# Kernel optimization log

Hardware: AMD Instinct MI355X
Metric: run time of the kernel (lower is better)

## Reference

```python
import jax, jax.numpy as jnp
import numpy as np

D = 1024      # embed_size
H = 16        # num_heads
NEXP = 8      # num_experts
TOPK = 3
THRESH = 0.05
COEF = 0.01
B, SQ, SKV = 4, 1024, 1024


def _ln(x, g, b, eps=1e-5):
    m = jnp.mean(x, axis=-1, keepdims=True)
    v = jnp.mean(jnp.square(x - m), axis=-1, keepdims=True)
    return (x - m) * jax.lax.rsqrt(v + eps) * g + b


def setup_inputs() -> dict:
    key = jax.random.key(0)
    ks = jax.random.split(key, 20)
    s = 0.02
    w = lambda k, shape: (jax.random.normal(k, shape, jnp.float32) * s)
    return {
        'query': jax.random.normal(ks[0], (B, SQ, D), jnp.float32),
        'key_value': jax.random.normal(ks[1], (B, SKV, D), jnp.float32),
        'Wq': w(ks[2], (D, D)), 'bq': jnp.zeros((D,), jnp.float32),
        'Wk': w(ks[3], (D, D)), 'bk': jnp.zeros((D,), jnp.float32),
        'Wv': w(ks[4], (D, D)), 'bv': jnp.zeros((D,), jnp.float32),
        'W_in': w(ks[5], (3 * D, D)), 'b_in': jnp.zeros((3 * D,), jnp.float32),
        'W_out': w(ks[6], (D, D)), 'b_out': jnp.zeros((D,), jnp.float32),
        'Wa': w(ks[7], (D, D)), 'ba': jnp.zeros((D,), jnp.float32),
        'ln1_g': jnp.ones((D,), jnp.float32), 'ln1_b': jnp.zeros((D,), jnp.float32),
        'Wg': w(ks[8], (D, NEXP)),
        'ew1': w(ks[9], (NEXP, D, 4 * D)), 'eb1': jnp.zeros((NEXP, 4 * D), jnp.float32),
        'ew2': w(ks[10], (NEXP, 4 * D, D)), 'eb2': jnp.zeros((NEXP, D), jnp.float32),
        'ln2_g': jnp.ones((D,), jnp.float32), 'ln2_b': jnp.zeros((D,), jnp.float32),
    }


def reference(query, key_value, Wq, bq, Wk, bk, Wv, bv, W_in, b_in, W_out, b_out,
              Wa, ba, ln1_g, ln1_b, Wg, ew1, eb1, ew2, eb2, ln2_g, ln2_b):
    Bq, Sq, _ = query.shape
    Skv = key_value.shape[1]
    Dh = D // H
    # outer Q/K/V linears (torch Linear: x @ W.T + b)
    q = query @ Wq.T + bq
    k = key_value @ Wk.T + bk
    v = key_value @ Wv.T + bv
    # nn.MultiheadAttention in-projection
    Wiq, Wik, Wiv = jnp.split(W_in, 3, axis=0)
    biq, bik, biv = jnp.split(b_in, 3)
    qh = (q @ Wiq.T + biq).reshape(Bq, Sq, H, Dh).transpose(0, 2, 1, 3)
    kh = (k @ Wik.T + bik).reshape(Bq, Skv, H, Dh).transpose(0, 2, 1, 3)
    vh = (v @ Wiv.T + biv).reshape(Bq, Skv, H, Dh).transpose(0, 2, 1, 3)
    scores = jnp.einsum('bhqd,bhkd->bhqk', qh, kh) / jnp.sqrt(jnp.float32(Dh))
    attn = jax.nn.softmax(scores, axis=-1)
    o = jnp.einsum('bhqk,bhkd->bhqd', attn, vh).transpose(0, 2, 1, 3).reshape(Bq, Sq, D)
    o = o @ W_out.T + b_out
    # adapt + residual + first_norm
    x = _ln(o @ Wa.T + ba + query, ln1_g, ln1_b)
    # ---- MoE: top-3 softmax gating, threshold on non-top-1 gates ----
    probs = jax.nn.softmax(x @ Wg, axis=-1)                 # [B,S,E]
    topv, topi = jax.lax.top_k(probs, TOPK)                  # [B,S,3]
    keep = jnp.concatenate([jnp.ones_like(topv[..., :1], bool),
                            topv[..., 1:] >= THRESH], axis=-1)
    topv = jnp.where(keep, topv, 0.0)
    combine = jnp.sum(jax.nn.one_hot(topi, NEXP, dtype=x.dtype) * topv[..., None], axis=-2)  # [B,S,E]
    moe_out = jnp.zeros_like(x)
    for e in range(NEXP):  # small fixed expert count
        h = jax.nn.gelu(x @ ew1[e] + eb1[e], approximate=False)
        moe_out = moe_out + combine[..., e:e + 1] * (h @ ew2[e] + eb2[e])
    # load-balance aux loss: E * sum(frac_routed * mean_prob) * coef
    fe = jnp.mean((combine > 0).astype(x.dtype), axis=(0, 1))
    me = jnp.mean(probs, axis=(0, 1))
    aux = COEF * NEXP * jnp.sum(fe * me)
    out = _ln(moe_out + x, ln2_g, ln2_b)
    return out, aux
```

## Files before the change

### kernel.cpp

```cpp
#include <hip/hip_runtime.h>
#include <math.h>

#define THRESH_C 0.05f
#define COEF_C   0.01f

typedef __bf16 bf16;
typedef __bf16 bf16x8 __attribute__((ext_vector_type(8)));
typedef __bf16 bf16x4 __attribute__((ext_vector_type(4)));
typedef float  f32x4  __attribute__((ext_vector_type(4)));

__device__ __forceinline__ void ld16(void* lds_base, const void* g) {
    __builtin_amdgcn_global_load_lds(
        (const __attribute__((address_space(1))) void*)g,
        (__attribute__((address_space(3))) void*)lds_base,
        16, 0, 0);
}

__device__ __forceinline__ int xcd_swz(int orig, int nwg) {
    int q = nwg >> 3, r = nwg & 7;
    int xcd = orig & 7, idx = orig >> 3;
    return (xcd < r ? xcd * (q + 1) : r * (q + 1) + (xcd - r) * q) + idx;
}

__global__ __launch_bounds__(256) void k_f32_to_split(const float* __restrict__ in,
                                                      bf16* __restrict__ hi,
                                                      bf16* __restrict__ lo, long n) {
    long i = ((long)blockIdx.x * 256 + threadIdx.x) * 4;
    if (i >= n) return;
    float4 v = *(const float4*)(in + i);
    bf16x4 h, l;
    h[0] = (bf16)v.x; l[0] = (bf16)(v.x - (float)h[0]);
    h[1] = (bf16)v.y; l[1] = (bf16)(v.y - (float)h[1]);
    h[2] = (bf16)v.z; l[2] = (bf16)(v.z - (float)h[2]);
    h[3] = (bf16)v.w; l[3] = (bf16)(v.w - (float)h[3]);
    *(bf16x4*)(hi + i) = h;
    *(bf16x4*)(lo + i) = l;
}

__global__ __launch_bounds__(256) void k_transpose4_split(const float* __restrict__ w0,
                                                          const float* __restrict__ w1,
                                                          const float* __restrict__ w2,
                                                          const float* __restrict__ w3,
                                                          bf16* __restrict__ oh,
                                                          bf16* __restrict__ ol) {
    __shared__ float t[64][65];
    int z = blockIdx.z;
    const float* in = (z == 0) ? w0 : (z == 1) ? w1 : (z == 2) ? w2 : w3;
    bf16* ohz = oh + (long)z * 1048576;
    bf16* olz = ol + (long)z * 1048576;
    int r0 = blockIdx.y * 64, c0 = blockIdx.x * 64;
    for (int i = threadIdx.x; i < 4096; i += 256) {
        int r = i >> 6, c = i & 63;
        t[r][c] = in[(long)(r0 + r) * 1024 + (c0 + c)];
    }
    __syncthreads();
    for (int i = threadIdx.x; i < 4096; i += 256) {
        int c = i >> 6, r = i & 63;
        float v = t[r][c];
        bf16 h = (bf16)v;
        long o = (long)(c0 + c) * 1024 + (r0 + r);
        ohz[o] = h;
        olz[o] = (bf16)(v - (float)h);
    }
}

__global__ __launch_bounds__(256) void k_transpose_ew(const float* __restrict__ in,
                                                      bf16* __restrict__ out,
                                                      int R, int C) {
    __shared__ bf16 t[64][65];
    const float* ib = in + (long)blockIdx.z * R * C;
    bf16* ob = out + (long)blockIdx.z * R * C;
    int r0 = blockIdx.y * 64, c0 = blockIdx.x * 64;
    for (int i = threadIdx.x; i < 4096; i += 256) {
        int r = i >> 6, c = i & 63;
        t[r][c] = (bf16)ib[(long)(r0 + r) * C + (c0 + c)];
    }
    __syncthreads();
    for (int i = threadIdx.x; i < 4096; i += 256) {
        int c = i >> 6, r = i & 63;
        ob[(long)(c0 + c) * R + (r0 + r)] = t[r][c];
    }
}

__global__ __launch_bounds__(256) void k_bias_fold4(const float* __restrict__ W_in,
                                                    const float* __restrict__ Wa,
                                                    const float* __restrict__ bq,
                                                    const float* __restrict__ bk,
                                                    const float* __restrict__ bv,
                                                    const float* __restrict__ b_out,
                                                    const float* __restrict__ b_in,
                                                    const float* __restrict__ ba,
                                                    float* __restrict__ y) {
    int z = blockIdx.y;
    const float* W  = (z < 3) ? (W_in + (long)z * 1048576) : Wa;
    const float* b1 = (z == 0) ? bq : (z == 1) ? bk : (z == 2) ? bv : b_out;
    const float* b2 = (z < 3) ? (b_in + z * 1024) : ba;
    int row = blockIdx.x * 4 + (threadIdx.x >> 6);
    int lane = threadIdx.x & 63;
    const float* wr = W + (long)row * 1024;
    float s = 0.f;
    for (int k = lane; k < 1024; k += 64) s += wr[k] * b1[k];
#pragma unroll
    for (int o = 32; o >= 1; o >>= 1) s += __shfl_xor(s, o);
    if (lane == 0) y[z * 1024 + row] = b2[row] + s;
}

enum { HP_SPLIT = 0, HP_F32 = 1, HP_SPLIT_HEADS = 2 };

template<int MODE>
__global__ __launch_bounds__(256)
void gemm_hp(const bf16* __restrict__ Ah, const bf16* __restrict__ Al, int lda, long sAz,
             const bf16* __restrict__ Bh, const bf16* __restrict__ Bl, int ldb, long sBz,
             void* __restrict__ Chv, bf16* __restrict__ Cl, int ldc, long sCz,
             const float* __restrict__ bias, float alpha, int M, int N, int K) {
    __shared__ alignas(16) bf16 sAh[128 * 32];
    __shared__ alignas(16) bf16 sAl[128 * 32];
    __shared__ alignas(16) bf16 sBh[128 * 32];
    __shared__ alignas(16) bf16 sBl[128 * 32];
    const int bm = blockIdx.y, bn = blockIdx.x, z = blockIdx.z;
    const int tid  = threadIdx.x;
    const int lane = tid & 63, wave = tid >> 6;
    const int quad = lane >> 4, l16 = lane & 15;
    const int wr = wave >> 1, wc = wave & 1;
    const int sr = tid >> 2;
    const int sc = (tid & 3) * 8;

    int arow0 = min(bm * 128 + sr, M - 1);
    int arow1 = min(bm * 128 + sr + 64, M - 1);
    int brow0 = min(bn * 128 + sr, N - 1);
    int brow1 = min(bn * 128 + sr + 64, N - 1);

    const bf16* pAh0 = Ah + (long)z * sAz + (long)arow0 * lda + sc;
    const bf16* pAh1 = Ah + (long)z * sAz + (long)arow1 * lda + sc;
    const bf16* pAl0 = Al + (long)z * sAz + (long)arow0 * lda + sc;
    const bf16* pAl1 = Al + (long)z * sAz + (long)arow1 * lda + sc;
    const bf16* pBh0 = Bh + (long)z * sBz + (long)brow0 * ldb + sc;
    const bf16* pBh1 = Bh + (long)z * sBz + (long)brow1 * ldb + sc;
    const bf16* pBl0 = Bl + (long)z * sBz + (long)brow0 * ldb + sc;
    const bf16* pBl1 = Bl + (long)z * sBz + (long)brow1 * ldb + sc;
    const int wo = wave << 9;

    f32x4 acc[4][4];
#pragma unroll
    for (int i = 0; i < 4; i++)
#pragma unroll
        for (int j = 0; j < 4; j++) acc[i][j] = (f32x4){0.f, 0.f, 0.f, 0.f};

    for (int k0 = 0; k0 < K; k0 += 32) {
        __syncthreads();
        ld16(sAh + wo,        pAh0 + k0);
        ld16(sAh + 2048 + wo, pAh1 + k0);
        ld16(sAl + wo,        pAl0 + k0);
        ld16(sAl + 2048 + wo, pAl1 + k0);
        ld16(sBh + wo,        pBh0 + k0);
        ld16(sBh + 2048 + wo, pBh1 + k0);
        ld16(sBl + wo,        pBl0 + k0);
        ld16(sBl + 2048 + wo, pBl1 + k0);
        __syncthreads();
        bf16x8 ah[4], al[4], bh[4], bl[4];
#pragma unroll
        for (int i = 0; i < 4; i++) {
            int ro = (wr * 64 + i * 16 + l16) * 32 + quad * 8;
            ah[i] = *(const bf16x8*)&sAh[ro];
            al[i] = *(const bf16x8*)&sAl[ro];
        }
#pragma unroll
        for (int j = 0; j < 4; j++) {
            int ro = (wc * 64 + j * 16 + l16) * 32 + quad * 8;
            bh[j] = *(const bf16x8*)&sBh[ro];
            bl[j] = *(const bf16x8*)&sBl[ro];
        }
#pragma unroll
        for (int i = 0; i < 4; i++)
#pragma unroll
            for (int j = 0; j < 4; j++) {
                acc[i][j] = __builtin_amdgcn_mfma_f32_16x16x32_bf16(al[i], bh[j], acc[i][j], 0, 0, 0);
                acc[i][j] = __builtin_amdgcn_mfma_f32_16x16x32_bf16(ah[i], bl[j], acc[i][j], 0, 0, 0);
                acc[i][j] = __builtin_amdgcn_mfma_f32_16x16x32_bf16(ah[i], bh[j], acc[i][j], 0, 0, 0);
            }
    }

#pragma unroll
    for (int i = 0; i < 4; i++) {
        int mbase = bm * 128 + wr * 64 + i * 16 + quad * 4;
#pragma unroll
        for (int j = 0; j < 4; j++) {
            int n = bn * 128 + wc * 64 + j * 16 + l16;
            if (n < N) {
                float bv = bias ? bias[n] : 0.f;
#pragma unroll
                for (int r = 0; r < 4; r++) {
                    int m = mbase + r;
                    if (m < M) {
                        float v = alpha * acc[i][j][r] + bv;
                        if (MODE == HP_SPLIT) {
                            long cidx = (long)z * sCz + (long)m * ldc + n;
                            bf16 h = (bf16)v;
                            ((bf16*)Chv)[cidx] = h;
                            Cl[cidx] = (bf16)(v - (float)h);
                        } else if (MODE == HP_F32) {
                            long cidx = (long)z * sCz + (long)m * ldc + n;
                            ((float*)Chv)[cidx] = v;
                        } else {
                            int slice = ((m >> 10) << 4) + (n >> 6);
                            long idx = (long)slice * 65536 + (long)(m & 1023) * 64 + (n & 63);
                            bf16 h = (bf16)v;
                            ((bf16*)Chv)[idx] = h;
                            Cl[idx] = (bf16)(v - (float)h);
                        }
                    }
                }
            }
        }
    }
}

__global__ __launch_bounds__(256)
void gemm_pv(const bf16* __restrict__ Ph, const bf16* __restrict__ Pl,
             const bf16* __restrict__ Vh, const bf16* __restrict__ Vl,
             bf16* __restrict__ Oh, bf16* __restrict__ Ol) {
    __shared__ alignas(16) bf16 sAh[128 * 32];
    __shared__ alignas(16) bf16 sAl[128 * 32];
    __shared__ alignas(16) bf16 sBh[64 * 32];
    __shared__ alignas(16) bf16 sBl[64 * 32];
    const int bm = blockIdx.x, z = blockIdx.y;
    const int tid = threadIdx.x, lane = tid & 63, wave = tid >> 6;
    const int quad = lane >> 4, l16 = lane & 15;
    const int wr = wave & 1, wc = wave >> 1;
    const int sr = tid >> 2, sc = (tid & 3) * 8;

    const bf16* pA0h = Ph + (long)z * 1048576 + (long)(bm * 128 + sr) * 1024 + sc;
    const bf16* pA1h = pA0h + 64 * 1024;
    const bf16* pA0l = Pl + (long)z * 1048576 + (long)(bm * 128 + sr) * 1024 + sc;
    const bf16* pA1l = pA0l + 64 * 1024;
    const bf16* pB0h = Vh + (long)z * 65536 + (long)sr * 1024 + sc;
    const bf16* pB0l = Vl + (long)z * 65536 + (long)sr * 1024 + sc;
    const int wo = wave << 9;

    f32x4 acc[4][2];
#pragma unroll
    for (int i = 0; i < 4; i++)
#pragma unroll
        for (int j = 0; j < 2; j++) acc[i][j] = (f32x4){0.f, 0.f, 0.f, 0.f};

    for (int k0 = 0; k0 < 1024; k0 += 32) {
        __syncthreads();
        ld16(sAh + wo,        pA0h + k0);
        ld16(sAh + 2048 + wo, pA1h + k0);
        ld16(sAl + wo,        pA0l + k0);
        ld16(sAl + 2048 + wo, pA1l + k0);
        ld16(sBh + wo, pB0h + k0);
        ld16(sBl + wo, pB0l + k0);
        __syncthreads();
        bf16x8 ah[4], al[4], bh[2], bl[2];
#pragma unroll
        for (int i = 0; i < 4; i++) {
            int ro = (wr * 64 + i * 16 + l16) * 32 + quad * 8;
            ah[i] = *(const bf16x8*)&sAh[ro];
            al[i] = *(const bf16x8*)&sAl[ro];
        }
#pragma unroll
        for (int j = 0; j < 2; j++) {
            int ro = (wc * 32 + j * 16 + l16) * 32 + quad * 8;
            bh[j] = *(const bf16x8*)&sBh[ro];
            bl[j] = *(const bf16x8*)&sBl[ro];
        }
#pragma unroll
        for (int i = 0; i < 4; i++)
#pragma unroll
            for (int j = 0; j < 2; j++) {
                acc[i][j] = __builtin_amdgcn_mfma_f32_16x16x32_bf16(al[i], bh[j], acc[i][j], 0, 0, 0);
                acc[i][j] = __builtin_amdgcn_mfma_f32_16x16x32_bf16(ah[i], bl[j], acc[i][j], 0, 0, 0);
                acc[i][j] = __builtin_amdgcn_mfma_f32_16x16x32_bf16(ah[i], bh[j], acc[i][j], 0, 0, 0);
            }
    }

#pragma unroll
    for (int i = 0; i < 4; i++) {
        int mbase = bm * 128 + wr * 64 + i * 16 + quad * 4;
#pragma unroll
        for (int j = 0; j < 2; j++) {
            int n = wc * 32 + j * 16 + l16;
#pragma unroll
            for (int r = 0; r < 4; r++) {
                int m = mbase + r;
                long idx = (long)z * 65536 + (long)m * 64 + n;
                float v = acc[i][j][r];
                bf16 h = (bf16)v;
                Oh[idx] = h;
                Ol[idx] = (bf16)(v - (float)h);
            }
        }
    }
}

__global__ __launch_bounds__(256)
void gemm_moe1(const bf16* __restrict__ Ae, const bf16* __restrict__ ew1t,
               const float* __restrict__ eb1, bf16* __restrict__ Hp,
               const int* __restrict__ counts, const int* __restrict__ bases,
               const int* __restrict__ tiles, const int* __restrict__ ntile) {
    const int wg = xcd_swz(blockIdx.x, gridDim.x);
    const int tile = wg >> 5;
    const int bn = wg & 31;
    if (tile >= ntile[0]) return;
    const int te = tiles[tile];
    const int e = te >> 16, bm = te & 0xffff;
    const int M = counts[e];
    const bf16* A = Ae + (long)bases[e] * 1024;
    const bf16* B = ew1t + (long)e * 4194304;
    bf16* C = Hp + (long)bases[e] * 4096;
    const float* bias = eb1 + e * 4096;

    __shared__ alignas(16) bf16 sA[128 * 32];
    __shared__ alignas(16) bf16 sB[128 * 32];
    const int tid  = threadIdx.x;
    const int lane = tid & 63, wave = tid >> 6;
    const int quad = lane >> 4, l16 = lane & 15;
    const int wr = wave >> 1, wc = wave & 1;
    const int sr = tid >> 2;
    const int sc = (tid & 3) * 8;

    int arow0 = min(bm * 128 + sr, M - 1);
    int arow1 = min(bm * 128 + sr + 64, M - 1);
    int brow0 = bn * 128 + sr;
    const bf16* pA0 = A + (long)arow0 * 1024 + sc;
    const bf16* pA1 = A + (long)arow1 * 1024 + sc;
    const bf16* pB0 = B + (long)brow0 * 1024 + sc;
    const bf16* pB1 = B + (long)(brow0 + 64) * 1024 + sc;
    const int wo = wave << 9;

    f32x4 acc[4][4];
#pragma unroll
    for (int i = 0; i < 4; i++)
#pragma unroll
        for (int j = 0; j < 4; j++) acc[i][j] = (f32x4){0.f, 0.f, 0.f, 0.f};

    for (int k0 = 0; k0 < 1024; k0 += 32) {
        __syncthreads();
        ld16(sA + wo,        pA0 + k0);
        ld16(sA + 2048 + wo, pA1 + k0);
        ld16(sB + wo,        pB0 + k0);
        ld16(sB + 2048 + wo, pB1 + k0);
        __syncthreads();
        bf16x8 af[4], bfr[4];
#pragma unroll
        for (int i = 0; i < 4; i++)
            af[i] = *(const bf16x8*)&sA[(wr * 64 + i * 16 + l16) * 32 + quad * 8];
#pragma unroll
        for (int j = 0; j < 4; j++)
            bfr[j] = *(const bf16x8*)&sB[(wc * 64 + j * 16 + l16) * 32 + quad * 8];
#pragma unroll
        for (int i = 0; i < 4; i++)
#pragma unroll
            for (int j = 0; j < 4; j++)
                acc[i][j] = __builtin_amdgcn_mfma_f32_16x16x32_bf16(af[i], bfr[j], acc[i][j], 0, 0, 0);
    }

#pragma unroll
    for (int i = 0; i < 4; i++) {
        int mbase = bm * 128 + wr * 64 + i * 16 + quad * 4;
#pragma unroll
        for (int j = 0; j < 4; j++) {
            int n = bn * 128 + wc * 64 + j * 16 + l16;
            float bv = bias[n];
#pragma unroll
            for (int r = 0; r < 4; r++) {
                int m = mbase + r;
                if (m < M) {
                    float v = acc[i][j][r] + bv;
                    float g = 0.5f * v * (1.f + erff(v * 0.70710678118654752f));
                    C[(long)m * 4096 + n] = (bf16)g;
                }
            }
        }
    }
}

__global__ __launch_bounds__(256)
void gemm_moe2(const bf16* __restrict__ Hp, const bf16* __restrict__ ew2t,
               float* __restrict__ Y,
               const int* __restrict__ counts, const int* __restrict__ bases,
               const int* __restrict__ tiles, const int* __restrict__ ntile) {
    const int wg = xcd_swz(blockIdx.x, gridDim.x);
    const int tile = wg >> 3;
    const int bn = wg & 7;
    if (tile >= ntile[0]) return;
    const int te = tiles[tile];
    const int e = te >> 16, bm = te & 0xffff;
    const int M = counts[e];
    const bf16* A = Hp + (long)bases[e] * 4096;
    const bf16* B = ew2t + (long)e * 4194304;
    float* C = Y + (long)bases[e] * 1024;

    __shared__ alignas(16) bf16 sA[128 * 32];
    __shared__ alignas(16) bf16 sB[128 * 32];
    const int tid  = threadIdx.x;
    const int lane = tid & 63, wave = tid >> 6;
    const int quad = lane >> 4, l16 = lane & 15;
    const int wr = wave >> 1, wc = wave & 1;
    const int sr = tid >> 2;
    const int sc = (tid & 3) * 8;

    int arow0 = min(bm * 128 + sr, M - 1);
    int arow1 = min(bm * 128 + sr + 64, M - 1);
    int brow0 = bn * 128 + sr;
    const bf16* pA0 = A + (long)arow0 * 4096 + sc;
    const bf16* pA1 = A + (long)arow1 * 4096 + sc;
    const bf16* pB0 = B + (long)brow0 * 4096 + sc;
    const bf16* pB1 = B + (long)(brow0 + 64) * 4096 + sc;
    const int wo = wave << 9;

    f32x4 acc[4][4];
#pragma unroll
    for (int i = 0; i < 4; i++)
#pragma unroll
        for (int j = 0; j < 4; j++) acc[i][j] = (f32x4){0.f, 0.f, 0.f, 0.f};

    for (int k0 = 0; k0 < 4096; k0 += 32) {
        __syncthreads();
        ld16(sA + wo,        pA0 + k0);
        ld16(sA + 2048 + wo, pA1 + k0);
        ld16(sB + wo,        pB0 + k0);
        ld16(sB + 2048 + wo, pB1 + k0);
        __syncthreads();
        bf16x8 af[4], bfr[4];
#pragma unroll
        for (int i = 0; i < 4; i++)
            af[i] = *(const bf16x8*)&sA[(wr * 64 + i * 16 + l16) * 32 + quad * 8];
#pragma unroll
        for (int j = 0; j < 4; j++)
            bfr[j] = *(const bf16x8*)&sB[(wc * 64 + j * 16 + l16) * 32 + quad * 8];
#pragma unroll
        for (int i = 0; i < 4; i++)
#pragma unroll
            for (int j = 0; j < 4; j++)
                acc[i][j] = __builtin_amdgcn_mfma_f32_16x16x32_bf16(af[i], bfr[j], acc[i][j], 0, 0, 0);
    }

#pragma unroll
    for (int i = 0; i < 4; i++) {
        int mbase = bm * 128 + wr * 64 + i * 16 + quad * 4;
#pragma unroll
        for (int j = 0; j < 4; j++) {
            int n = bn * 128 + wc * 64 + j * 16 + l16;
#pragma unroll
            for (int r = 0; r < 4; r++) {
                int m = mbase + r;
                if (m < M) C[(long)m * 1024 + n] = acc[i][j][r];
            }
        }
    }
}

__global__ __launch_bounds__(256) void k_vsplit(const bf16* __restrict__ VH_h,
                                                const bf16* __restrict__ VH_l,
                                                bf16* __restrict__ VT_h,
                                                bf16* __restrict__ VT_l) {
    __shared__ bf16 th[64][65];
    __shared__ bf16 tl[64][65];
    int s = blockIdx.y, q0 = blockIdx.x * 64;
    int b = s >> 4, h = s & 15;
    long ibase = ((long)(b * 1024 + q0)) * 1024 + h * 64;
    for (int i = threadIdx.x; i < 4096; i += 256) {
        int q = i >> 6, d = i & 63;
        th[q][d] = VH_h[ibase + (long)q * 1024 + d];
        tl[q][d] = VH_l[ibase + (long)q * 1024 + d];
    }
    __syncthreads();
    long obase = (long)s * 65536 + q0;
    for (int i = threadIdx.x; i < 4096; i += 256) {
        int d = i >> 6, q = i & 63;
        VT_h[obase + (long)d * 1024 + q] = th[q][d];
        VT_l[obase + (long)d * 1024 + q] = tl[q][d];
    }
}

__global__ __launch_bounds__(256) void k_ocopy(const bf16* __restrict__ Op_h,
                                               const bf16* __restrict__ Op_l,
                                               bf16* __restrict__ O_h,
                                               bf16* __restrict__ O_l) {
    int t = blockIdx.x * 4 + (threadIdx.x >> 6);
    int lane = threadIdx.x & 63;
    int b = t >> 10, q = t & 1023;
    int h = lane >> 2, dd = (lane & 3) * 16;
    long src = ((long)(b * 16 + h)) * 65536 + (long)q * 64 + dd;
    long dst = (long)t * 1024 + h * 64 + dd;
    *(bf16x8*)(O_h + dst)     = *(const bf16x8*)(Op_h + src);
    *(bf16x8*)(O_h + dst + 8) = *(const bf16x8*)(Op_h + src + 8);
    *(bf16x8*)(O_l + dst)     = *(const bf16x8*)(Op_l + src);
    *(bf16x8*)(O_l + dst + 8) = *(const bf16x8*)(Op_l + src + 8);
}

__global__ __launch_bounds__(256) void k_gather(const bf16* __restrict__ Xb,
                                                const int* __restrict__ tok,
                                                const int* __restrict__ counts,
                                                const int* __restrict__ bases,
                                                bf16* __restrict__ Ae) {
    int e = blockIdx.y;
    int cnt = counts[e];
    long base = bases[e];
    for (int i = blockIdx.x; i < cnt; i += gridDim.x) {
        int t = tok[e * 4096 + i];
        const bf16x4* src = (const bf16x4*)(Xb + (long)t * 1024);
        bf16x4* dst = (bf16x4*)(Ae + (base + i) * 1024);
        dst[threadIdx.x] = src[threadIdx.x];
    }
}

__global__ __launch_bounds__(256) void k_softmax_ip(bf16* __restrict__ Sh,
                                                    bf16* __restrict__ Sl) {
    int row = blockIdx.x * 4 + (threadIdx.x >> 6);
    int lane = threadIdx.x & 63;
    long o = (long)row * 1024 + lane * 16;
    bf16x8 h0 = *(const bf16x8*)(Sh + o), h1 = *(const bf16x8*)(Sh + o + 8);
    bf16x8 l0 = *(const bf16x8*)(Sl + o), l1 = *(const bf16x8*)(Sl + o + 8);
    float v[16];
#pragma unroll
    for (int i = 0; i < 8; i++) {
        v[i] = (float)h0[i] + (float)l0[i];
        v[8 + i] = (float)h1[i] + (float)l1[i];
    }
    float mx = v[0];
#pragma unroll
    for (int i = 1; i < 16; i++) mx = fmaxf(mx, v[i]);
#pragma unroll
    for (int of = 32; of >= 1; of >>= 1) mx = fmaxf(mx, __shfl_xor(mx, of));
    float s = 0.f;
#pragma unroll
    for (int i = 0; i < 16; i++) { v[i] = expf(v[i] - mx); s += v[i]; }
#pragma unroll
    for (int of = 32; of >= 1; of >>= 1) s += __shfl_xor(s, of);
    float inv = 1.f / s;
#pragma unroll
    for (int i = 0; i < 8; i++) {
        float a = v[i] * inv;
        h0[i] = (bf16)a; l0[i] = (bf16)(a - (float)h0[i]);
        float b = v[8 + i] * inv;
        h1[i] = (bf16)b; l1[i] = (bf16)(b - (float)h1[i]);
    }
    *(bf16x8*)(Sh + o) = h0;  *(bf16x8*)(Sh + o + 8) = h1;
    *(bf16x8*)(Sl + o) = l0;  *(bf16x8*)(Sl + o + 8) = l1;
}

__global__ __launch_bounds__(256) void k_ln(const float* __restrict__ xin,
                                            const float* __restrict__ resid,
                                            const float* __restrict__ g,
                                            const float* __restrict__ bb,
                                            float* __restrict__ outf,
                                            bf16* __restrict__ outb) {
    int row = blockIdx.x * 4 + (threadIdx.x >> 6);
    int lane = threadIdx.x & 63;
    long base = (long)row * 1024 + lane * 16;
    float v[16];
#pragma unroll
    for (int i = 0; i < 16; i += 4) {
        f32x4 a = *(const f32x4*)(xin + base + i);
        if (resid) { f32x4 r4 = *(const f32x4*)(resid + base + i); a += r4; }
        v[i] = a[0]; v[i + 1] = a[1]; v[i + 2] = a[2]; v[i + 3] = a[3];
    }
    float s = 0.f;
#pragma unroll
    for (int i = 0; i < 16; i++) s += v[i];
#pragma unroll
    for (int o = 32; o >= 1; o >>= 1) s += __shfl_xor(s, o);
    float mean = s * (1.f / 1024.f);
    float vs = 0.f;
#pragma unroll
    for (int i = 0; i < 16; i++) { float d = v[i] - mean; vs += d * d; }
#pragma unroll
    for (int o = 32; o >= 1; o >>= 1) vs += __shfl_xor(vs, o);
    float inv = 1.f / sqrtf(vs * (1.f / 1024.f) + 1e-5f);
    const float* gp = g + lane * 16;
    const float* bp = bb + lane * 16;
#pragma unroll
    for (int i = 0; i < 16; i++) {
        float o = (v[i] - mean) * inv * gp[i] + bp[i];
        if (outf) outf[base + i] = o;
        if (outb) outb[base + i] = (bf16)o;
    }
}

__global__ __launch_bounds__(256) void k_moe_ln(const float* __restrict__ Y,
                                                const int* __restrict__ pos,
                                                const float* __restrict__ combine,
                                                const float* __restrict__ eb2,
                                                const float* __restrict__ resid,
                                                const float* __restrict__ g,
                                                const float* __restrict__ bb,
                                                float* __restrict__ outf) {
    int row = blockIdx.x * 4 + (threadIdx.x >> 6);
    int lane = threadIdx.x & 63;
    long base = (long)row * 1024 + lane * 16;
    float v[16];
#pragma unroll
    for (int i = 0; i < 16; i += 4) {
        f32x4 a = *(const f32x4*)(resid + base + i);
        v[i] = a[0]; v[i + 1] = a[1]; v[i + 2] = a[2]; v[i + 3] = a[3];
    }
    for (int e = 0; e < 8; e++) {
        int p = pos[row * 8 + e];
        if (p >= 0) {
            float c = combine[row * 8 + e];
            const float* yr = Y + (long)p * 1024 + lane * 16;
            const float* br = eb2 + e * 1024 + lane * 16;
#pragma unroll
            for (int i = 0; i < 16; i += 4) {
                f32x4 y4 = *(const f32x4*)(yr + i);
                f32x4 b4 = *(const f32x4*)(br + i);
                v[i]     += c * (y4[0] + b4[0]);
                v[i + 1] += c * (y4[1] + b4[1]);
                v[i + 2] += c * (y4[2] + b4[2]);
                v[i + 3] += c * (y4[3] + b4[3]);
            }
        }
    }
    float s = 0.f;
#pragma unroll
    for (int i = 0; i < 16; i++) s += v[i];
#pragma unroll
    for (int o = 32; o >= 1; o >>= 1) s += __shfl_xor(s, o);
    float mean = s * (1.f / 1024.f);
    float vs = 0.f;
#pragma unroll
    for (int i = 0; i < 16; i++) { float d = v[i] - mean; vs += d * d; }
#pragma unroll
    for (int o = 32; o >= 1; o >>= 1) vs += __shfl_xor(vs, o);
    float inv = 1.f / sqrtf(vs * (1.f / 1024.f) + 1e-5f);
    const float* gp = g + lane * 16;
    const float* bp = bb + lane * 16;
#pragma unroll
    for (int i = 0; i < 16; i++)
        outf[base + i] = (v[i] - mean) * inv * gp[i] + bp[i];
}

__global__ __launch_bounds__(256) void k_gate(const float* __restrict__ X,
                                              const float* __restrict__ Wg,
                                              float* __restrict__ combine,
                                              float* __restrict__ partials) {
    __shared__ float sm[16];
    if (threadIdx.x < 16) sm[threadIdx.x] = 0.f;
    __syncthreads();
    int t = blockIdx.x * 4 + (threadIdx.x >> 6);
    int lane = threadIdx.x & 63;
    const float* x = X + (long)t * 1024;
    float acc[8] = {0.f, 0.f, 0.f, 0.f, 0.f, 0.f, 0.f, 0.f};
    for (int i = lane; i < 1024; i += 64) {
        float xv = x[i];
        const float* w = Wg + i * 8;
#pragma unroll
        for (int e = 0; e < 8; e++) acc[e] += xv * w[e];
    }
#pragma unroll
    for (int e = 0; e < 8; e++)
#pragma unroll
        for (int o = 32; o >= 1; o >>= 1) acc[e] += __shfl_xor(acc[e], o);
    if (lane == 0) {
        float mx = acc[0];
#pragma unroll
        for (int e = 1; e < 8; e++) mx = fmaxf(mx, acc[e]);
        float p[8], s = 0.f;
#pragma unroll
        for (int e = 0; e < 8; e++) { p[e] = expf(acc[e] - mx); s += p[e]; }
        float invs = 1.f / s;
#pragma unroll
        for (int e = 0; e < 8; e++) p[e] *= invs;
        float b1 = -1.f, b2 = -1.f, b3 = -1.f; int i1 = 0, i2 = 0, i3 = 0;
#pragma unroll
        for (int e = 0; e < 8; e++) {
            float pe = p[e];
            if (pe > b1)      { b3 = b2; i3 = i2; b2 = b1; i2 = i1; b1 = pe; i1 = e; }
            else if (pe > b2) { b3 = b2; i3 = i2; b2 = pe; i2 = e; }
            else if (pe > b3) { b3 = pe; i3 = e; }
        }
        float c[8] = {0.f, 0.f, 0.f, 0.f, 0.f, 0.f, 0.f, 0.f};
        c[i1] = b1;
        if (b2 >= THRESH_C) c[i2] = b2;
        if (b3 >= THRESH_C) c[i3] = b3;
        float* co = combine + (long)t * 8;
#pragma unroll
        for (int e = 0; e < 8; e++) co[e] = c[e];
#pragma unroll
        for (int e = 0; e < 8; e++) {
            atomicAdd(&sm[e], p[e]);
            if (c[e] > 0.f) atomicAdd(&sm[8 + e], 1.f);
        }
    }
    __syncthreads();
    if (threadIdx.x < 16) partials[(long)blockIdx.x * 16 + threadIdx.x] = sm[threadIdx.x];
}

__global__ __launch_bounds__(256) void k_route(const float* __restrict__ combine,
                                               int* __restrict__ counts,
                                               int* __restrict__ bases,
                                               int* __restrict__ tok,
                                               int* __restrict__ pos,
                                               int* __restrict__ tiles,
                                               int* __restrict__ ntile) {
    __shared__ int scan[256];
    int tid = threadIdx.x;
    int mybase = 0;
    int nt = 0;
    for (int e = 0; e < 8; e++) {
        int pred[16]; int cnt = 0;
#pragma unroll
        for (int j = 0; j < 16; j++) {
            int t = tid * 16 + j;
            pred[j] = combine[t * 8 + e] > 0.f ? 1 : 0;
            cnt += pred[j];
        }
        scan[tid] = cnt;
        __syncthreads();
        for (int off = 1; off < 256; off <<= 1) {
            int v = (tid >= off) ? scan[tid - off] : 0;
            __syncthreads();
            scan[tid] += v;
            __syncthreads();
        }
        int start = scan[tid] - cnt;
        int total = scan[255];
        int o = e * 4096 + start;
        int gp = mybase + start;
#pragma unroll
        for (int j = 0; j < 16; j++) {
            int t = tid * 16 + j;
            if (pred[j]) { tok[o++] = t; pos[t * 8 + e] = gp++; }
            else pos[t * 8 + e] = -1;
        }
        if (tid == 0) {
            counts[e] = total; bases[e] = mybase;
            int nte = (total + 127) >> 7;
            for (int b = 0; b < nte; b++) tiles[nt++] = (e << 16) | b;
        }
        mybase += total;
        __syncthreads();
    }
    if (tid == 0) ntile[0] = nt;
}

__global__ __launch_bounds__(256) void k_aux(const float* __restrict__ partials, int nblocks,
                                             float* __restrict__ auxout) {
    __shared__ float red[256];
    int tid = threadIdx.x;
    int e = tid & 15, grp = tid >> 4;
    float s = 0.f;
    for (int b = grp; b < nblocks; b += 16) s += partials[(long)b * 16 + e];
    red[tid] = s;
    __syncthreads();
    if (grp == 0) {
        float tot = 0.f;
        for (int g2 = 0; g2 < 16; g2++) tot += red[g2 * 16 + e];
        red[tid] = tot;
    }
    __syncthreads();
    if (tid == 0) {
        float s2 = 0.f;
        for (int e2 = 0; e2 < 8; e2++)
            s2 += (red[8 + e2] * (1.f / 4096.f)) * (red[e2] * (1.f / 4096.f));
        auxout[0] = COEF_C * 8.f * s2;
    }
}

extern "C" void kernel_launch(void* const* d_in, const int* in_sizes, int n_in,
                              void* d_out, int out_size, void* d_ws, size_t ws_size,
                              hipStream_t stream) {
    const float* query     = (const float*)d_in[0];
    const float* key_value = (const float*)d_in[1];
    const float* Wq   = (const float*)d_in[2];
    const float* bq   = (const float*)d_in[3];
    const float* Wk   = (const float*)d_in[4];
    const float* bk   = (const float*)d_in[5];
    const float* Wv   = (const float*)d_in[6];
    const float* bv   = (const float*)d_in[7];
    const float* W_in = (const float*)d_in[8];
    const float* b_in = (const float*)d_in[9];
    const float* W_out = (const float*)d_in[10];
    const float* b_out = (const float*)d_in[11];
    const float* Wa   = (const float*)d_in[12];
    const float* ba   = (const float*)d_in[13];
    const float* ln1_g = (const float*)d_in[14];
    const float* ln1_b = (const float*)d_in[15];
    const float* Wg   = (const float*)d_in[16];
    const float* ew1  = (const float*)d_in[17];
    const float* eb1  = (const float*)d_in[18];
    const float* ew2  = (const float*)d_in[19];
    const float* eb2  = (const float*)d_in[20];
    const float* ln2_g = (const float*)d_in[21];
    const float* ln2_b = (const float*)d_in[22];

    const size_t MBY = 1ull << 20;
    const long MB1 = 1024L * 1024L;
    char* ws = (char*)d_ws;

    bf16* Sh   = (bf16*)(ws + 0 * MBY);
    bf16* Sl   = (bf16*)(ws + 64 * MBY);
    bf16* ew1t = (bf16*)(ws + 0 * MBY);
    bf16* ew2t = (bf16*)(ws + 64 * MBY);
    bf16* WAll_h = (bf16*)(ws + 128 * MBY);
    bf16* WAll_l = (bf16*)(ws + 136 * MBY);
    bf16* WT_h   = (bf16*)(ws + 144 * MBY);
    bf16* WT_l   = (bf16*)(ws + 152 * MBY);
    bf16* Xq_h  = (bf16*)(ws + 160 * MBY), *Xq_l  = (bf16*)(ws + 168 * MBY);
    bf16* Xkv_h = (bf16*)(ws + 176 * MBY), *Xkv_l = (bf16*)(ws + 184 * MBY);
    bf16* O_h  = (bf16*)(ws + 160 * MBY), *O_l  = (bf16*)(ws + 168 * MBY);
    bf16* QHp_h = (bf16*)(ws + 192 * MBY), *QHp_l = (bf16*)(ws + 200 * MBY);
    bf16* KHp_h = (bf16*)(ws + 208 * MBY), *KHp_l = (bf16*)(ws + 216 * MBY);
    bf16* VH_h  = (bf16*)(ws + 224 * MBY), *VH_l  = (bf16*)(ws + 232 * MBY);
    bf16* VTp_h = (bf16*)(ws + 240 * MBY), *VTp_l = (bf16*)(ws + 248 * MBY);
    bf16* Op_h  = (bf16*)(ws + 256 * MBY), *Op_l  = (bf16*)(ws + 264 * MBY);
    float* Xf   = (float*)(ws + 256 * MBY);
    float* Af   = (float*)(ws + 272 * MBY);
    bf16* Ae      = (bf16*)(ws + 128 * MBY);
    bf16* Hp      = (bf16*)(ws + 152 * MBY);
    float* Yp     = (float*)(ws + 272 * MBY);
    bf16* Xb   = (bf16*)(ws + 320 * MBY);
    bf16* Weff_h = (bf16*)(ws + 328 * MBY);
    bf16* Weff_l = (bf16*)(ws + 336 * MBY);
    float* combine  = (float*)(ws + 344 * MBY);
    float* partials = (float*)(ws + 344 * MBY + 128 * 1024);
    float* beff     = (float*)(ws + 344 * MBY + 192 * 1024);
    int*   counts   = (int*)  (ws + 344 * MBY + 212 * 1024);
    int*   bases    = (int*)  (ws + 344 * MBY + 213 * 1024);
    int*   tok      = (int*)  (ws + 344 * MBY + 214 * 1024);
    int*   pos      = (int*)  (ws + 344 * MBY + 342 * 1024);
    int*   tiles    = (int*)  (ws + 344 * MBY + 472 * 1024);
    int*   ntile    = tiles + 128;

    dim3 blk(256);

    k_f32_to_split<<<4096, blk, 0, stream>>>(query, Xq_h, Xq_l, 4L * MB1);
    k_f32_to_split<<<4096, blk, 0, stream>>>(key_value, Xkv_h, Xkv_l, 4L * MB1);
    k_f32_to_split<<<3072, blk, 0, stream>>>(W_in, WAll_h, WAll_l, 3L * MB1);
    k_f32_to_split<<<1024, blk, 0, stream>>>(Wa, WAll_h + 3 * MB1, WAll_l + 3 * MB1, MB1);
    k_transpose4_split<<<dim3(16, 16, 4), blk, 0, stream>>>(Wq, Wk, Wv, W_out, WT_h, WT_l);
    k_bias_fold4<<<dim3(256, 4), blk, 0, stream>>>(W_in, Wa, bq, bk, bv, b_out, b_in, ba, beff);

    gemm_hp<HP_SPLIT><<<dim3(8, 8, 4), blk, 0, stream>>>(
        WAll_h, WAll_l, 1024, MB1, WT_h, WT_l, 1024, MB1,
        Weff_h, Weff_l, 1024, MB1, nullptr, 1.f, 1024, 1024, 1024);

    dim3 gP(8, 32, 1);
    gemm_hp<HP_SPLIT_HEADS><<<gP, blk, 0, stream>>>(Xq_h, Xq_l, 1024, 0, Weff_h, Weff_l, 1024, 0,
                                                    QHp_h, QHp_l, 0, 0, beff, 1.f, 4096, 1024, 1024);
    gemm_hp<HP_SPLIT_HEADS><<<gP, blk, 0, stream>>>(Xkv_h, Xkv_l, 1024, 0, Weff_h + MB1, Weff_l + MB1, 1024, 0,
                                                    KHp_h, KHp_l, 0, 0, beff + 1024, 1.f, 4096, 1024, 1024);
    gemm_hp<HP_SPLIT><<<gP, blk, 0, stream>>>(Xkv_h, Xkv_l, 1024, 0, Weff_h + 2 * MB1, Weff_l + 2 * MB1, 1024, 0,
                                              VH_h, VH_l, 1024, 0, beff + 2048, 1.f, 4096, 1024, 1024);
    k_vsplit<<<dim3(16, 64), blk, 0, stream>>>(VH_h, VH_l, VTp_h, VTp_l);

    for (int half = 0; half < 2; half++) {
        long so = (long)half * 32 * 65536;
        gemm_hp<HP_SPLIT><<<dim3(8, 8, 32), blk, 0, stream>>>(
            QHp_h + so, QHp_l + so, 64, 65536,
            KHp_h + so, KHp_l + so, 64, 65536,
            Sh, Sl, 1024, MB1, nullptr, 0.125f, 1024, 1024, 64);
        k_softmax_ip<<<8192, blk, 0, stream>>>(Sh, Sl);
        gemm_pv<<<dim3(8, 32), blk, 0, stream>>>(Sh, Sl, VTp_h + so, VTp_l + so,
                                                 Op_h + so, Op_l + so);
    }
    k_ocopy<<<1024, blk, 0, stream>>>(Op_h, Op_l, O_h, O_l);

    gemm_hp<HP_F32><<<gP, blk, 0, stream>>>(O_h, O_l, 1024, 0, Weff_h + 3 * MB1, Weff_l + 3 * MB1, 1024, 0,
                                            Af, nullptr, 1024, 0, beff + 3072, 1.f, 4096, 1024, 1024);
    k_ln<<<1024, blk, 0, stream>>>(Af, query, ln1_g, ln1_b, Xf, Xb);
    k_gate<<<1024, blk, 0, stream>>>(Xf, Wg, combine, partials);
    k_route<<<1, blk, 0, stream>>>(combine, counts, bases, tok, pos, tiles, ntile);
    k_gather<<<dim3(512, 8), blk, 0, stream>>>(Xb, tok, counts, bases, Ae);

    k_transpose_ew<<<dim3(64, 16, 8), blk, 0, stream>>>(ew1, ew1t, 1024, 4096);
    k_transpose_ew<<<dim3(16, 64, 8), blk, 0, stream>>>(ew2, ew2t, 4096, 1024);

    gemm_moe1<<<dim3(104 * 32), blk, 0, stream>>>(Ae, ew1t, eb1, Hp, counts, bases, tiles, ntile);
    gemm_moe2<<<dim3(104 * 8), blk, 0, stream>>>(Hp, ew2t, Yp, counts, bases, tiles, ntile);

    k_moe_ln<<<1024, blk, 0, stream>>>(Yp, pos, combine, eb2, Xf, ln2_g, ln2_b, (float*)d_out);
    k_aux<<<1, blk, 0, stream>>>(partials, 1024, (float*)d_out + (out_size - 1));
}
```

Measured before the change: 1.608 ms.

## Overlap global-to-LDS loads with MFMA in GEMMs and batch Q/K projections

The MoE GEMMs and the PV GEMM get double-buffered LDS tiles, so the next K-slice is loaded while the current one feeds the MFMAs. The split-precision GEMM keeps a single buffer but now issues the next slice's loads right after reading fragments into registers, before its MFMAs, rather than between two barriers. The Q and K projections are merged into one launch over a z dimension, using a new per-z bias stride and output offset. This targets load latency exposed between barriers and one launch's overhead, at the cost of doubled LDS use, which may lower occupancy, and reliance on the assumed workspace stride between the Q and KV buffers.

```diff
diff --git a/kernel.cpp b/kernel.cpp
--- a/kernel.cpp
+++ b/kernel.cpp
@@ -112,7 +112,7 @@
 void gemm_hp(const bf16* __restrict__ Ah, const bf16* __restrict__ Al, int lda, long sAz,
              const bf16* __restrict__ Bh, const bf16* __restrict__ Bl, int ldb, long sBz,
              void* __restrict__ Chv, bf16* __restrict__ Cl, int ldc, long sCz,
-             const float* __restrict__ bias, float alpha, int M, int N, int K) {
+             const float* __restrict__ bias, long sbz, float alpha, int M, int N, int K) {
     __shared__ alignas(16) bf16 sAh[128 * 32];
     __shared__ alignas(16) bf16 sAl[128 * 32];
     __shared__ alignas(16) bf16 sBh[128 * 32];
@@ -146,17 +146,17 @@
 #pragma unroll
         for (int j = 0; j < 4; j++) acc[i][j] = (f32x4){0.f, 0.f, 0.f, 0.f};
 
+    ld16(sAh + wo,        pAh0);
+    ld16(sAh + 2048 + wo, pAh1);
+    ld16(sAl + wo,        pAl0);
+    ld16(sAl + 2048 + wo, pAl1);
+    ld16(sBh + wo,        pBh0);
+    ld16(sBh + 2048 + wo, pBh1);
+    ld16(sBl + wo,        pBl0);
+    ld16(sBl + 2048 + wo, pBl1);
+    __syncthreads();
+
     for (int k0 = 0; k0 < K; k0 += 32) {
-        __syncthreads();
-        ld16(sAh + wo,        pAh0 + k0);
-        ld16(sAh + 2048 + wo, pAh1 + k0);
-        ld16(sAl + wo,        pAl0 + k0);
-        ld16(sAl + 2048 + wo, pAl1 + k0);
-        ld16(sBh + wo,        pBh0 + k0);
-        ld16(sBh + 2048 + wo, pBh1 + k0);
-        ld16(sBl + wo,        pBl0 + k0);
-        ld16(sBl + 2048 + wo, pBl1 + k0);
-        __syncthreads();
         bf16x8 ah[4], al[4], bh[4], bl[4];
 #pragma unroll
         for (int i = 0; i < 4; i++) {
@@ -169,6 +169,18 @@
             int ro = (wc * 64 + j * 16 + l16) * 32 + quad * 8;
             bh[j] = *(const bf16x8*)&sBh[ro];
             bl[j] = *(const bf16x8*)&sBl[ro];
+        }
+        __syncthreads();
+        int kn = k0 + 32;
+        if (kn < K) {
+            ld16(sAh + wo,        pAh0 + kn);
+            ld16(sAh + 2048 + wo, pAh1 + kn);
+            ld16(sAl + wo,        pAl0 + kn);
+            ld16(sAl + 2048 + wo, pAl1 + kn);
+            ld16(sBh + wo,        pBh0 + kn);
+            ld16(sBh + 2048 + wo, pBh1 + kn);
+            ld16(sBl + wo,        pBl0 + kn);
+            ld16(sBl + 2048 + wo, pBl1 + kn);
         }
 #pragma unroll
         for (int i = 0; i < 4; i++)
@@ -178,6 +190,7 @@
                 acc[i][j] = __builtin_amdgcn_mfma_f32_16x16x32_bf16(ah[i], bl[j], acc[i][j], 0, 0, 0);
                 acc[i][j] = __builtin_amdgcn_mfma_f32_16x16x32_bf16(ah[i], bh[j], acc[i][j], 0, 0, 0);
             }
+        __syncthreads();
     }
 
 #pragma unroll
@@ -187,7 +200,7 @@
         for (int j = 0; j < 4; j++) {
             int n = bn * 128 + wc * 64 + j * 16 + l16;
             if (n < N) {
-                float bv = bias ? bias[n] : 0.f;
+                float bv = bias ? bias[(long)z * sbz + n] : 0.f;
 #pragma unroll
                 for (int r = 0; r < 4; r++) {
                     int m = mbase + r;
@@ -203,7 +216,7 @@
                             ((float*)Chv)[cidx] = v;
                         } else {
                             int slice = ((m >> 10) << 4) + (n >> 6);
-                            long idx = (long)slice * 65536 + (long)(m & 1023) * 64 + (n & 63);
+                            long idx = (long)z * sCz + (long)slice * 65536 + (long)(m & 1023) * 64 + (n & 63);
                             bf16 h = (bf16)v;
                             ((bf16*)Chv)[idx] = h;
                             Cl[idx] = (bf16)(v - (float)h);
@@ -219,10 +232,10 @@
 void gemm_pv(const bf16* __restrict__ Ph, const bf16* __restrict__ Pl,
              const bf16* __restrict__ Vh, const bf16* __restrict__ Vl,
              bf16* __restrict__ Oh, bf16* __restrict__ Ol) {
-    __shared__ alignas(16) bf16 sAh[128 * 32];
-    __shared__ alignas(16) bf16 sAl[128 * 32];
-    __shared__ alignas(16) bf16 sBh[64 * 32];
-    __shared__ alignas(16) bf16 sBl[64 * 32];
+    __shared__ alignas(16) bf16 sAh[2][128 * 32];
+    __shared__ alignas(16) bf16 sAl[2][128 * 32];
+    __shared__ alignas(16) bf16 sBh[2][64 * 32];
+    __shared__ alignas(16) bf16 sBl[2][64 * 32];
     const int bm = blockIdx.x, z = blockIdx.y;
     const int tid = threadIdx.x, lane = tid & 63, wave = tid >> 6;
     const int quad = lane >> 4, l16 = lane & 15;
@@ -243,27 +256,39 @@
 #pragma unroll
         for (int j = 0; j < 2; j++) acc[i][j] = (f32x4){0.f, 0.f, 0.f, 0.f};
 
+    ld16(sAh[0] + wo,        pA0h);
+    ld16(sAh[0] + 2048 + wo, pA1h);
+    ld16(sAl[0] + wo,        pA0l);
+    ld16(sAl[0] + 2048 + wo, pA1l);
+    ld16(sBh[0] + wo, pB0h);
+    ld16(sBl[0] + wo, pB0l);
+    __syncthreads();
+
+    int cur = 0;
     for (int k0 = 0; k0 < 1024; k0 += 32) {
-        __syncthreads();
-        ld16(sAh + wo,        pA0h + k0);
-        ld16(sAh + 2048 + wo, pA1h + k0);
-        ld16(sAl + wo,        pA0l + k0);
-        ld16(sAl + 2048 + wo, pA1l + k0);
-        ld16(sBh + wo, pB0h + k0);
-        ld16(sBl + wo, pB0l + k0);
-        __syncthreads();
+        int kn = k0 + 32;
+        if (kn < 1024) {
+            ld16(sAh[cur ^ 1] + wo,        pA0h + kn);
+            ld16(sAh[cur ^ 1] + 2048 + wo, pA1h + kn);
+            ld16(sAl[cur ^ 1] + wo,        pA0l + kn);
+            ld16(sAl[cur ^ 1] + 2048 + wo, pA1l + kn);
+            ld16(sBh[cur ^ 1] + wo, pB0h + kn);
+            ld16(sBl[cur ^ 1] + wo, pB0l + kn);
+        }
+        const bf16* cAh = sAh[cur]; const bf16* cAl = sAl[cur];
+        const bf16* cBh = sBh[cur]; const bf16* cBl = sBl[cur];
         bf16x8 ah[4], al[4], bh[2], bl[2];
 #pragma unroll
         for (int i = 0; i < 4; i++) {
             int ro = (wr * 64 + i * 16 + l16) * 32 + quad * 8;
-            ah[i] = *(const bf16x8*)&sAh[ro];
-            al[i] = *(const bf16x8*)&sAl[ro];
+            ah[i] = *(const bf16x8*)&cAh[ro];
+            al[i] = *(const bf16x8*)&cAl[ro];
         }
 #pragma unroll
         for (int j = 0; j < 2; j++) {
             int ro = (wc * 32 + j * 16 + l16) * 32 + quad * 8;
-            bh[j] = *(const bf16x8*)&sBh[ro];
-            bl[j] = *(const bf16x8*)&sBl[ro];
+            bh[j] = *(const bf16x8*)&cBh[ro];
+            bl[j] = *(const bf16x8*)&cBl[ro];
         }
 #pragma unroll
         for (int i = 0; i < 4; i++)
@@ -273,6 +298,8 @@
                 acc[i][j] = __builtin_amdgcn_mfma_f32_16x16x32_bf16(ah[i], bl[j], acc[i][j], 0, 0, 0);
                 acc[i][j] = __builtin_amdgcn_mfma_f32_16x16x32_bf16(ah[i], bh[j], acc[i][j], 0, 0, 0);
             }
+        __syncthreads();
+        cur ^= 1;
     }
 
 #pragma unroll
@@ -311,8 +338,8 @@
     bf16* C = Hp + (long)bases[e] * 4096;
     const float* bias = eb1 + e * 4096;
 
-    __shared__ alignas(16) bf16 sA[128 * 32];
-    __shared__ alignas(16) bf16 sB[128 * 32];
+    __shared__ alignas(16) bf16 sA[2][128 * 32];
+    __shared__ alignas(16) bf16 sB[2][128 * 32];
     const int tid  = threadIdx.x;
     const int lane = tid & 63, wave = tid >> 6;
     const int quad = lane >> 4, l16 = lane & 15;
@@ -335,25 +362,36 @@
 #pragma unroll
         for (int j = 0; j < 4; j++) acc[i][j] = (f32x4){0.f, 0.f, 0.f, 0.f};
 
+    ld16(sA[0] + wo,        pA0);
+    ld16(sA[0] + 2048 + wo, pA1);
+    ld16(sB[0] + wo,        pB0);
+    ld16(sB[0] + 2048 + wo, pB1);
+    __syncthreads();
+
+    int cur = 0;
     for (int k0 = 0; k0 < 1024; k0 += 32) {
-        __syncthreads();
-        ld16(sA + wo,        pA0 + k0);
-        ld16(sA + 2048 + wo, pA1 + k0);
-        ld16(sB + wo,        pB0 + k0);
-        ld16(sB + 2048 + wo, pB1 + k0);
-        __syncthreads();
+        int kn = k0 + 32;
+        if (kn < 1024) {
+            ld16(sA[cur ^ 1] + wo,        pA0 + kn);
+            ld16(sA[cur ^ 1] + 2048 + wo, pA1 + kn);
+            ld16(sB[cur ^ 1] + wo,        pB0 + kn);
+            ld16(sB[cur ^ 1] + 2048 + wo, pB1 + kn);
+        }
+        const bf16* cA = sA[cur]; const bf16* cB = sB[cur];
         bf16x8 af[4], bfr[4];
 #pragma unroll
         for (int i = 0; i < 4; i++)
-            af[i] = *(const bf16x8*)&sA[(wr * 64 + i * 16 + l16) * 32 + quad * 8];
+            af[i] = *(const bf16x8*)&cA[(wr * 64 + i * 16 + l16) * 32 + quad * 8];
 #pragma unroll
         for (int j = 0; j < 4; j++)
-            bfr[j] = *(const bf16x8*)&sB[(wc * 64 + j * 16 + l16) * 32 + quad * 8];
+            bfr[j] = *(const bf16x8*)&cB[(wc * 64 + j * 16 + l16) * 32 + quad * 8];
 #pragma unroll
         for (int i = 0; i < 4; i++)
 #pragma unroll
             for (int j = 0; j < 4; j++)
                 acc[i][j] = __builtin_amdgcn_mfma_f32_16x16x32_bf16(af[i], bfr[j], acc[i][j], 0, 0, 0);
+        __syncthreads();
+        cur ^= 1;
     }
 
 #pragma unroll
@@ -392,8 +430,8 @@
     const bf16* B = ew2t + (long)e * 4194304;
     float* C = Y + (long)bases[e] * 1024;
 
-    __shared__ alignas(16) bf16 sA[128 * 32];
-    __shared__ alignas(16) bf16 sB[128 * 32];
+    __shared__ alignas(16) bf16 sA[2][128 * 32];
+    __shared__ alignas(16) bf16 sB[2][128 * 32];
     const int tid  = threadIdx.x;
     const int lane = tid & 63, wave = tid >> 6;
     const int quad = lane >> 4, l16 = lane & 15;
@@ -416,25 +454,36 @@
 #pragma unroll
         for (int j = 0; j < 4; j++) acc[i][j] = (f32x4){0.f, 0.f, 0.f, 0.f};
 
+    ld16(sA[0] + wo,        pA0);
+    ld16(sA[0] + 2048 + wo, pA1);
+    ld16(sB[0] + wo,        pB0);
+    ld16(sB[0] + 2048 + wo, pB1);
+    __syncthreads();
+
+    int cur = 0;
     for (int k0 = 0; k0 < 4096; k0 += 32) {
-        __syncthreads();
-        ld16(sA + wo,        pA0 + k0);
-        ld16(sA + 2048 + wo, pA1 + k0);
-        ld16(sB + wo,        pB0 + k0);
-        ld16(sB + 2048 + wo, pB1 + k0);
-        __syncthreads();
+        int kn = k0 + 32;
+        if (kn < 4096) {
+            ld16(sA[cur ^ 1] + wo,        pA0 + kn);
+            ld16(sA[cur ^ 1] + 2048 + wo, pA1 + kn);
+            ld16(sB[cur ^ 1] + wo,        pB0 + kn);
+            ld16(sB[cur ^ 1] + 2048 + wo, pB1 + kn);
+        }
+        const bf16* cA = sA[cur]; const bf16* cB = sB[cur];
         bf16x8 af[4], bfr[4];
 #pragma unroll
         for (int i = 0; i < 4; i++)
-            af[i] = *(const bf16x8*)&sA[(wr * 64 + i * 16 + l16) * 32 + quad * 8];
+            af[i] = *(const bf16x8*)&cA[(wr * 64 + i * 16 + l16) * 32 + quad * 8];
 #pragma unroll
         for (int j = 0; j < 4; j++)
-            bfr[j] = *(const bf16x8*)&sB[(wc * 64 + j * 16 + l16) * 32 + quad * 8];
+            bfr[j] = *(const bf16x8*)&cB[(wc * 64 + j * 16 + l16) * 32 + quad * 8];
 #pragma unroll
         for (int i = 0; i < 4; i++)
 #pragma unroll
             for (int j = 0; j < 4; j++)
                 acc[i][j] = __builtin_amdgcn_mfma_f32_16x16x32_bf16(af[i], bfr[j], acc[i][j], 0, 0, 0);
+        __syncthreads();
+        cur ^= 1;
     }
 
 #pragma unroll
@@ -836,15 +885,14 @@
 
     gemm_hp<HP_SPLIT><<<dim3(8, 8, 4), blk, 0, stream>>>(
         WAll_h, WAll_l, 1024, MB1, WT_h, WT_l, 1024, MB1,
-        Weff_h, Weff_l, 1024, MB1, nullptr, 1.f, 1024, 1024, 1024);
-
-    dim3 gP(8, 32, 1);
-    gemm_hp<HP_SPLIT_HEADS><<<gP, blk, 0, stream>>>(Xq_h, Xq_l, 1024, 0, Weff_h, Weff_l, 1024, 0,
-                                                    QHp_h, QHp_l, 0, 0, beff, 1.f, 4096, 1024, 1024);
-    gemm_hp<HP_SPLIT_HEADS><<<gP, blk, 0, stream>>>(Xkv_h, Xkv_l, 1024, 0, Weff_h + MB1, Weff_l + MB1, 1024, 0,
-                                                    KHp_h, KHp_l, 0, 0, beff + 1024, 1.f, 4096, 1024, 1024);
-    gemm_hp<HP_SPLIT><<<gP, blk, 0, stream>>>(Xkv_h, Xkv_l, 1024, 0, Weff_h + 2 * MB1, Weff_l + 2 * MB1, 1024, 0,
-                                              VH_h, VH_l, 1024, 0, beff + 2048, 1.f, 4096, 1024, 1024);
+        Weff_h, Weff_l, 1024, MB1, nullptr, 0, 1.f, 1024, 1024, 1024);
+
+    gemm_hp<HP_SPLIT_HEADS><<<dim3(8, 32, 2), blk, 0, stream>>>(
+        Xq_h, Xq_l, 1024, 8 * MB1, Weff_h, Weff_l, 1024, MB1,
+        QHp_h, QHp_l, 0, 8 * MB1, beff, 1024, 1.f, 4096, 1024, 1024);
+    gemm_hp<HP_SPLIT><<<dim3(8, 32, 1), blk, 0, stream>>>(
+        Xkv_h, Xkv_l, 1024, 0, Weff_h + 2 * MB1, Weff_l + 2 * MB1, 1024, 0,
+        VH_h, VH_l, 1024, 0, beff + 2048, 0, 1.f, 4096, 1024, 1024);
     k_vsplit<<<dim3(16, 64), blk, 0, stream>>>(VH_h, VH_l, VTp_h, VTp_l);
 
     for (int half = 0; half < 2; half++) {
@@ -852,15 +900,16 @@
         gemm_hp<HP_SPLIT><<<dim3(8, 8, 32), blk, 0, stream>>>(
             QHp_h + so, QHp_l + so, 64, 65536,
             KHp_h + so, KHp_l + so, 64, 65536,
-            Sh, Sl, 1024, MB1, nullptr, 0.125f, 1024, 1024, 64);
+            Sh, Sl, 1024, MB1, nullptr, 0, 0.125f, 1024, 1024, 64);
         k_softmax_ip<<<8192, blk, 0, stream>>>(Sh, Sl);
         gemm_pv<<<dim3(8, 32), blk, 0, stream>>>(Sh, Sl, VTp_h + so, VTp_l + so,
                                                  Op_h + so, Op_l + so);
     }
     k_ocopy<<<1024, blk, 0, stream>>>(Op_h, Op_l, O_h, O_l);
 
-    gemm_hp<HP_F32><<<gP, blk, 0, stream>>>(O_h, O_l, 1024, 0, Weff_h + 3 * MB1, Weff_l + 3 * MB1, 1024, 0,
-                                            Af, nullptr, 1024, 0, beff + 3072, 1.f, 4096, 1024, 1024);
+    gemm_hp<HP_F32><<<dim3(8, 32, 1), blk, 0, stream>>>(
+        O_h, O_l, 1024, 0, Weff_h + 3 * MB1, Weff_l + 3 * MB1, 1024, 0,
+        Af, nullptr, 1024, 0, beff + 3072, 0, 1.f, 4096, 1024, 1024);
     k_ln<<<1024, blk, 0, stream>>>(Af, query, ln1_g, ln1_b, Xf, Xb);
     k_gate<<<1024, blk, 0, stream>>>(Xf, Wg, combine, partials);
     k_route<<<1, blk, 0, stream>>>(combine, counts, bases, tok, pos, tiles, ntile);
```

Result: faster. 1.552 ms (-3.5%).
